# Kernel tuning notes

Hardware: AMD Instinct MI355X
Metric: run time of the kernel (lower is better)

## Reference

```python
import jax, jax.numpy as jnp
import numpy as np

NEG_SLOPE = 0.2  # DGL GATConv default leaky_relu slope
N_LIG, E_LIG = 10000, 80000
N_REC, E_REC = 30000, 480000
B = 32  # graphs per batch


def setup_inputs() -> dict:
    key = jax.random.key(0)
    ks = jax.random.split(key, 32)
    d = {}
    d["x_lig"] = jax.random.normal(ks[0], (N_LIG, 64), jnp.float32)
    d["src_lig"] = jax.random.randint(ks[1], (E_LIG,), 0, N_LIG, jnp.int32)
    d["dst_lig"] = jax.random.randint(ks[2], (E_LIG,), 0, N_LIG, jnp.int32)
    d["gid_lig"] = jnp.sort(jax.random.randint(ks[3], (N_LIG,), 0, B, jnp.int32))
    d["x_rec"] = jax.random.normal(ks[4], (N_REC, 64), jnp.float32)
    d["src_rec"] = jax.random.randint(ks[5], (E_REC,), 0, N_REC, jnp.int32)
    d["dst_rec"] = jax.random.randint(ks[6], (E_REC,), 0, N_REC, jnp.int32)
    d["gid_rec"] = jnp.sort(jax.random.randint(ks[7], (N_REC,), 0, B, jnp.int32))
    s = 0.1
    # GAT layer 1 (lig): 64 -> 10 heads x 64 ; layer 2: 64 -> 1 head x 128
    d["W1l"] = s * jax.random.normal(ks[8], (64, 10 * 64), jnp.float32)
    d["al1l"] = s * jax.random.normal(ks[9], (10, 64), jnp.float32)
    d["ar1l"] = s * jax.random.normal(ks[10], (10, 64), jnp.float32)
    d["b1l"] = jnp.zeros((10, 64), jnp.float32)
    d["W2l"] = s * jax.random.normal(ks[11], (64, 128), jnp.float32)
    d["al2l"] = s * jax.random.normal(ks[12], (1, 128), jnp.float32)
    d["ar2l"] = s * jax.random.normal(ks[13], (1, 128), jnp.float32)
    d["b2l"] = jnp.zeros((1, 128), jnp.float32)
    d["W1r"] = s * jax.random.normal(ks[14], (64, 10 * 64), jnp.float32)
    d["al1r"] = s * jax.random.normal(ks[15], (10, 64), jnp.float32)
    d["ar1r"] = s * jax.random.normal(ks[16], (10, 64), jnp.float32)
    d["b1r"] = jnp.zeros((10, 64), jnp.float32)
    d["W2r"] = s * jax.random.normal(ks[17], (64, 128), jnp.float32)
    d["al2r"] = s * jax.random.normal(ks[18], (1, 128), jnp.float32)
    d["ar2r"] = s * jax.random.normal(ks[19], (1, 128), jnp.float32)
    d["b2r"] = jnp.zeros((1, 128), jnp.float32)
    d["W_lin1"] = s * jax.random.normal(ks[20], (256, 128), jnp.float32)
    d["b_lin1"] = jnp.zeros((128,), jnp.float32)
    d["W_lin2"] = s * jax.random.normal(ks[21], (128, 1), jnp.float32)
    d["b_lin2"] = jnp.zeros((1,), jnp.float32)
    return d


def gat_conv(x, src, dst, W, al, ar, b, num_nodes):
    # DGL GATConv (eval mode: dropouts off). al/ar: [H, D]
    H, D = al.shape
    h = (x @ W).reshape(num_nodes, H, D)          # [N, H, D]
    el = jnp.einsum("nhd,hd->nh", h, al)          # [N, H]
    er = jnp.einsum("nhd,hd->nh", h, ar)
    e = jax.nn.leaky_relu(el[src] + er[dst], NEG_SLOPE)   # [E, H]
    # edge softmax over incoming edges of each dst node
    emax = jax.ops.segment_max(e, dst, num_segments=num_nodes)
    ex = jnp.exp(e - emax[dst])
    denom = jax.ops.segment_sum(ex, dst, num_segments=num_nodes)
    alpha = ex / denom[dst]                       # [E, H]
    msg = alpha[:, :, None] * h[src]              # [E, H, D]
    out = jax.ops.segment_sum(msg, dst, num_segments=num_nodes)
    return out + b[None]                          # [N, H, D]


def branch(x, src, dst, gid, W1, al1, ar1, b1, W2, al2, ar2, b2):
    n = x.shape[0]
    h = jax.nn.relu(gat_conv(x, src, dst, W1, al1, ar1, b1, n)).sum(axis=1)  # sum heads -> [N, 64]
    h = jax.nn.relu(gat_conv(h, src, dst, W2, al2, ar2, b2, n))[:, 0, :]     # [N, 128]
    return jax.ops.segment_max(h, gid, num_segments=B)                       # max readout [B, 128]


def reference(x_lig, src_lig, dst_lig, gid_lig, x_rec, src_rec, dst_rec, gid_rec,
              W1l, al1l, ar1l, b1l, W2l, al2l, ar2l, b2l,
              W1r, al1r, ar1r, b1r, W2r, al2r, ar2r, b2r,
              W_lin1, b_lin1, W_lin2, b_lin2):
    hlig = branch(x_lig, src_lig, dst_lig, gid_lig, W1l, al1l, ar1l, b1l, W2l, al2l, ar2l, b2l)
    hrec = branch(x_rec, src_rec, dst_rec, gid_rec, W1r, al1r, ar1r, b1r, W2r, al2r, ar2r, b2r)
    h = jnp.concatenate([hlig, hrec], axis=-1)    # [B, 256]
    h = jax.nn.relu(h @ W_lin1 + b_lin1)
    h = jax.nn.relu(h @ W_lin2 + b_lin2)
    return h.flatten()                            # [B]
```

## Files before the change

kernel.cpp:

```cpp
#include <hip/hip_runtime.h>

#define LRELU(x) fmaxf((x), 0.2f*(x))
#define ZPAD(f) ((f) + 4*((f)>>6))

static inline int cdiv(int a, int b) { return (a + b - 1) / b; }

template<int H, int DH>
__global__ void prep_wal2_kernel(const float* __restrict__ WA, const float* __restrict__ alA,
                                 const float* __restrict__ arA, float* __restrict__ walA,
                                 float* __restrict__ warA, int nbA,
                                 const float* __restrict__ WB, const float* __restrict__ alB,
                                 const float* __restrict__ arB, float* __restrict__ walB,
                                 float* __restrict__ warB) {
  constexpr int K = 64;
  constexpr int HD = H * DH;
  const float *W, *al, *ar; float *wal, *war; int bid;
  if (blockIdx.x < (unsigned)nbA) { W=WA; al=alA; ar=arA; wal=walA; war=warA; bid=blockIdx.x; }
  else { W=WB; al=alB; ar=arB; wal=walB; war=warB; bid=blockIdx.x-nbA; }
  const int wv = threadIdx.x >> 6, lane = threadIdx.x & 63;
  const int o = bid * (blockDim.x >> 6) + wv;
  if (o >= H * K) return;
  const int h = o / K, k = o - h * K;
  float pl = 0.f, pr = 0.f;
#pragma unroll
  for (int j = 0; j < DH / 64; j++) {
    int d = j * 64 + lane;
    float w = W[(size_t)k * HD + h * DH + d];
    pl += w * al[h * DH + d];
    pr += w * ar[h * DH + d];
  }
#pragma unroll
  for (int off = 32; off >= 1; off >>= 1) {
    pl += __shfl_xor(pl, off);
    pr += __shfl_xor(pr, off);
  }
  if (lane == 0) { wal[o] = pl; war[o] = pr; }
}

__global__ void elr10_2_kernel(const float* __restrict__ xA, const float* __restrict__ walA,
                               const float* __restrict__ warA, float* __restrict__ elA,
                               float* __restrict__ erA, int NA, int nbA,
                               const float* __restrict__ xB, const float* __restrict__ walB,
                               const float* __restrict__ warB, float* __restrict__ elB,
                               float* __restrict__ erB, int NB) {
  const float *x, *wal, *war; float *el, *er; int N, bid;
  if (blockIdx.x < (unsigned)nbA) { x=xA; wal=walA; war=warA; el=elA; er=erA; N=NA; bid=blockIdx.x; }
  else { x=xB; wal=walB; war=warB; el=elB; er=erB; N=NB; bid=blockIdx.x-nbA; }
  const int wv = threadIdx.x >> 6, lane = threadIdx.x & 63;
  const int n = bid * (blockDim.x >> 6) + wv;
  if (n >= N) return;
  const float xv = x[(size_t)n * 64 + lane];
#pragma unroll
  for (int h = 0; h < 10; h++) {
    float pl = xv * wal[h * 64 + lane];
    float pr = xv * war[h * 64 + lane];
#pragma unroll
    for (int off = 32; off >= 1; off >>= 1) {
      pl += __shfl_xor(pl, off);
      pr += __shfl_xor(pr, off);
    }
    if (lane == 0) { el[(size_t)n * 10 + h] = pl; er[(size_t)n * 10 + h] = pr; }
  }
}

__global__ void deg2_kernel(const int* __restrict__ dstA, int* __restrict__ degA, int EA, int nbA,
                            const int* __restrict__ dstB, int* __restrict__ degB, int EB) {
  const int* dst; int* deg; int E, t;
  if (blockIdx.x < (unsigned)nbA) { dst=dstA; deg=degA; E=EA; t=blockIdx.x*256+threadIdx.x; }
  else { dst=dstB; deg=degB; E=EB; t=(blockIdx.x-nbA)*256+threadIdx.x; }
  if (t < E) atomicAdd(&deg[dst[t]], 1);
}

__global__ void rowptr2_kernel(const int* __restrict__ degA, int* __restrict__ rpA,
                               int* __restrict__ curA, int* __restrict__ cntA, int NA, int nbA,
                               const int* __restrict__ degB, int* __restrict__ rpB,
                               int* __restrict__ curB, int* __restrict__ cntB, int NB) {
  const int* deg; int *rp, *cur, *cnt; int N, t;
  if (blockIdx.x < (unsigned)nbA) { deg=degA; rp=rpA; cur=curA; cnt=cntA; N=NA; t=blockIdx.x*256+threadIdx.x; }
  else { deg=degB; rp=rpB; cur=curB; cnt=cntB; N=NB; t=(blockIdx.x-nbA)*256+threadIdx.x; }
  int lane = threadIdx.x & 63;
  int v = (t < N) ? deg[t] : 0;
  int x = v;
#pragma unroll
  for (int off = 1; off < 64; off <<= 1) {
    int y = __shfl_up(x, off);
    if (lane >= off) x += y;
  }
  int total = __shfl(x, 63);
  int base = 0;
  if (lane == 0 && total > 0) base = atomicAdd(cnt, total);
  base = __shfl(base, 0);
  int excl = base + x - v;
  if (t < N) { rp[t] = excl; cur[t] = excl; }
}

__global__ void scatter_ex2_kernel(
    const int* __restrict__ srcA, const int* __restrict__ dstA, int* __restrict__ curA,
    int* __restrict__ outA, const float* __restrict__ elA, const float* __restrict__ erA,
    float* __restrict__ exA, int* __restrict__ eslotA, int EA, int nbA,
    const int* __restrict__ srcB, const int* __restrict__ dstB, int* __restrict__ curB,
    int* __restrict__ outB, const float* __restrict__ elB, const float* __restrict__ erB,
    float* __restrict__ exB, int* __restrict__ eslotB, int EB) {
  const int *src, *dst; int *cur, *out, *eslot; const float *el, *er; float *ex; int E, t;
  if (blockIdx.x < (unsigned)nbA) { src=srcA; dst=dstA; cur=curA; out=outA; el=elA; er=erA; ex=exA; eslot=eslotA; E=EA; t=blockIdx.x*256+threadIdx.x; }
  else { src=srcB; dst=dstB; cur=curB; out=outB; el=elB; er=erB; ex=exB; eslot=eslotB; E=EB; t=(blockIdx.x-nbA)*256+threadIdx.x; }
  if (t >= E) return;
  const int s = src[t], d = dst[t];
  const int slot = atomicAdd(&cur[d], 1);
  out[slot] = s;
  eslot[t] = slot;
  const float2* elv = (const float2*)el;
  const float2* erv = (const float2*)er;
  float2* exv = (float2*)ex;
#pragma unroll
  for (int j = 0; j < 5; j++) {
    float2 a = elv[(size_t)s * 5 + j];
    float2 b = erv[(size_t)d * 5 + j];
    float2 e;
    e.x = __expf(LRELU(a.x + b.x));
    e.y = __expf(LRELU(a.y + b.y));
    exv[(size_t)slot * 5 + j] = e;
  }
}

__global__ void ex2_2_kernel(const int* __restrict__ srcA, const int* __restrict__ dstA,
                             const int* __restrict__ eslotA, const float* __restrict__ el2A,
                             const float* __restrict__ er2A, float* __restrict__ ex2A,
                             int EA, int nbA,
                             const int* __restrict__ srcB, const int* __restrict__ dstB,
                             const int* __restrict__ eslotB, const float* __restrict__ el2B,
                             const float* __restrict__ er2B, float* __restrict__ ex2B, int EB) {
  const int *src, *dst, *eslot; const float *el2, *er2; float *ex2; int E, t;
  if (blockIdx.x < (unsigned)nbA) { src=srcA; dst=dstA; eslot=eslotA; el2=el2A; er2=er2A; ex2=ex2A; E=EA; t=blockIdx.x*256+threadIdx.x; }
  else { src=srcB; dst=dstB; eslot=eslotB; el2=el2B; er2=er2B; ex2=ex2B; E=EB; t=(blockIdx.x-nbA)*256+threadIdx.x; }
  if (t >= E) return;
  ex2[eslot[t]] = __expf(LRELU(el2[src[t]] + er2[dst[t]]));
}

__global__ void aggr_z10_2_kernel(const int* __restrict__ rpA, const int* __restrict__ degA,
                                  const int* __restrict__ srcsA, const float* __restrict__ xA,
                                  const float* __restrict__ exA, float* __restrict__ zA,
                                  int NA, int nbA,
                                  const int* __restrict__ rpB, const int* __restrict__ degB,
                                  const int* __restrict__ srcsB, const float* __restrict__ xB,
                                  const float* __restrict__ exB, float* __restrict__ zB, int NB) {
  const int *rp, *degp, *srcs; const float *x, *ex; float *z; int N, bid;
  if (blockIdx.x < (unsigned)nbA) { rp=rpA; degp=degA; srcs=srcsA; x=xA; ex=exA; z=zA; N=NA; bid=blockIdx.x; }
  else { rp=rpB; degp=degB; srcs=srcsB; x=xB; ex=exB; z=zB; N=NB; bid=blockIdx.x-nbA; }
  const int wv = threadIdx.x >> 6, lane = threadIdx.x & 63;
  const int n = bid * (blockDim.x >> 6) + wv;
  if (n >= N) return;
  const int beg = rp[n], dg = degp[n];
  const float2* exv = (const float2*)ex;
  float den[10], acc[10];
#pragma unroll
  for (int h = 0; h < 10; h++) { den[h] = 0.f; acc[h] = 0.f; }
  int i = 0;
  for (; i + 1 < dg; i += 2) {
    int s0 = srcs[beg + i], s1 = srcs[beg + i + 1];
    float xv0 = x[(size_t)s0 * 64 + lane];
    float xv1 = x[(size_t)s1 * 64 + lane];
    float e0[10], e1[10];
#pragma unroll
    for (int j = 0; j < 5; j++) {
      float2 a = exv[(size_t)(beg + i) * 5 + j];
      float2 c = exv[(size_t)(beg + i + 1) * 5 + j];
      e0[2 * j] = a.x; e0[2 * j + 1] = a.y;
      e1[2 * j] = c.x; e1[2 * j + 1] = c.y;
    }
#pragma unroll
    for (int h = 0; h < 10; h++) {
      den[h] += e0[h] + e1[h];
      acc[h] = fmaf(e0[h], xv0, fmaf(e1[h], xv1, acc[h]));
    }
  }
  if (i < dg) {
    int s0 = srcs[beg + i];
    float xv0 = x[(size_t)s0 * 64 + lane];
#pragma unroll
    for (int j = 0; j < 5; j++) {
      float2 a = exv[(size_t)(beg + i) * 5 + j];
      den[2 * j] += a.x;
      den[2 * j + 1] += a.y;
      acc[2 * j] = fmaf(a.x, xv0, acc[2 * j]);
      acc[2 * j + 1] = fmaf(a.y, xv0, acc[2 * j + 1]);
    }
  }
#pragma unroll
  for (int h = 0; h < 10; h++)
    z[(size_t)n * 640 + h * 64 + lane] = (dg > 0) ? acc[h] / den[h] : 0.f;
}

__global__ void aggr_z1_2_kernel(const int* __restrict__ rpA, const int* __restrict__ degA,
                                 const int* __restrict__ srcsA, const float* __restrict__ hA,
                                 const float* __restrict__ exA, float* __restrict__ zA,
                                 int NA, int nbA,
                                 const int* __restrict__ rpB, const int* __restrict__ degB,
                                 const int* __restrict__ srcsB, const float* __restrict__ hB,
                                 const float* __restrict__ exB, float* __restrict__ zB, int NB) {
  const int *rp, *degp, *srcs; const float *hin, *ex; float *z; int N, bid;
  if (blockIdx.x < (unsigned)nbA) { rp=rpA; degp=degA; srcs=srcsA; hin=hA; ex=exA; z=zA; N=NA; bid=blockIdx.x; }
  else { rp=rpB; degp=degB; srcs=srcsB; hin=hB; ex=exB; z=zB; N=NB; bid=blockIdx.x-nbA; }
  const int wv = threadIdx.x >> 6, lane = threadIdx.x & 63;
  const int n = bid * (blockDim.x >> 6) + wv;
  if (n >= N) return;
  const int beg = rp[n], dg = degp[n];
  float den = 0.f, acc = 0.f;
  int i = 0;
  for (; i + 1 < dg; i += 2) {
    int s0 = srcs[beg + i], s1 = srcs[beg + i + 1];
    float e0 = ex[beg + i], e1 = ex[beg + i + 1];
    den += e0 + e1;
    acc = fmaf(e0, hin[(size_t)s0 * 64 + lane], fmaf(e1, hin[(size_t)s1 * 64 + lane], acc));
  }
  if (i < dg) {
    int s0 = srcs[beg + i];
    float e0 = ex[beg + i];
    den += e0;
    acc = fmaf(e0, hin[(size_t)s0 * 64 + lane], acc);
  }
  z[(size_t)n * 64 + lane] = (dg > 0) ? acc / den : 0.f;
}

__global__ void gemm_sumheads2_kernel(
    const float* __restrict__ zA, const float* __restrict__ WA, const float* __restrict__ bA,
    const float* __restrict__ wal2A, const float* __restrict__ war2A, float* __restrict__ h1A,
    float* __restrict__ el2A, float* __restrict__ er2A, int NA, int nbA,
    const float* __restrict__ zB, const float* __restrict__ WB, const float* __restrict__ bB,
    const float* __restrict__ wal2B, const float* __restrict__ war2B, float* __restrict__ h1B,
    float* __restrict__ el2B, float* __restrict__ er2B, int NB) {
  constexpr int NPB = 16;
  __shared__ float zs[NPB][680];
  const float *z, *W, *bb, *wal2, *war2; float *h1sum, *el2, *er2; int N, tile;
  if (blockIdx.x < (unsigned)nbA) { z=zA; W=WA; bb=bA; wal2=wal2A; war2=war2A; h1sum=h1A; el2=el2A; er2=er2A; N=NA; tile=blockIdx.x; }
  else { z=zB; W=WB; bb=bB; wal2=wal2B; war2=war2B; h1sum=h1B; el2=el2B; er2=er2B; N=NB; tile=blockIdx.x-nbA; }
  const int f = threadIdx.x;
  const int n0 = tile * NPB;
  const int pf = ZPAD(f);
#pragma unroll
  for (int i = 0; i < NPB; i++) {
    int n = n0 + i;
    zs[i][pf] = (n < N) ? z[(size_t)n * 640 + f] : 0.f;
  }
  __syncthreads();
  const int f4 = f % 160;
  const int ng = f / 160;
  const int head = f4 >> 4;
  const int base = 68 * head;
  float acc[4][4];
#pragma unroll
  for (int i = 0; i < 4; i++)
#pragma unroll
    for (int j = 0; j < 4; j++) acc[i][j] = 0.f;
  const float4* W4 = (const float4*)W;
  float4 wn[4];
#pragma unroll
  for (int j = 0; j < 4; j++) wn[j] = W4[(size_t)j * 160 + f4];
#pragma unroll
  for (int k4 = 0; k4 < 16; k4++) {
    float4 wc[4];
#pragma unroll
    for (int j = 0; j < 4; j++) wc[j] = wn[j];
    if (k4 < 15) {
#pragma unroll
      for (int j = 0; j < 4; j++) wn[j] = W4[(size_t)(4 * (k4 + 1) + j) * 160 + f4];
    }
    float4 zq[4];
#pragma unroll
    for (int i = 0; i < 4; i++)
      zq[i] = *(const float4*)&zs[ng * 4 + i][base + 4 * k4];
#pragma unroll
    for (int j4 = 0; j4 < 4; j4++) {
      const float4 w4 = wc[j4];
#pragma unroll
      for (int i = 0; i < 4; i++) {
        const float zv = j4 == 0 ? zq[i].x : j4 == 1 ? zq[i].y : j4 == 2 ? zq[i].z : zq[i].w;
        acc[i][0] = fmaf(zv, w4.x, acc[i][0]);
        acc[i][1] = fmaf(zv, w4.y, acc[i][1]);
        acc[i][2] = fmaf(zv, w4.z, acc[i][2]);
        acc[i][3] = fmaf(zv, w4.w, acc[i][3]);
      }
    }
  }
  const float4 b4 = ((const float4*)bb)[f4];
  __syncthreads();
#pragma unroll
  for (int i = 0; i < 4; i++) {
    float* row = &zs[ng * 4 + i][ZPAD(4 * f4)];
    row[0] = fmaxf(acc[i][0] + b4.x, 0.f);
    row[1] = fmaxf(acc[i][1] + b4.y, 0.f);
    row[2] = fmaxf(acc[i][2] + b4.z, 0.f);
    row[3] = fmaxf(acc[i][3] + b4.w, 0.f);
  }
  __syncthreads();
  const int lane = threadIdx.x & 63;
  for (int idx = threadIdx.x; idx < NPB * 64; idx += 640) {
    const int i = idx >> 6, d = idx & 63;
    float s = 0.f;
#pragma unroll
    for (int h = 0; h < 10; h++) s += zs[i][68 * h + d];
    const int n = n0 + i;
    float pl = s * wal2[d], pr = s * war2[d];
#pragma unroll
    for (int off = 32; off >= 1; off >>= 1) {
      pl += __shfl_xor(pl, off);
      pr += __shfl_xor(pr, off);
    }
    if (n < N) {
      h1sum[(size_t)n * 64 + d] = s;
      if (lane == 0) { el2[n] = pl; er2[n] = pr; }
    }
  }
}

__global__ void gemm2_readout3_kernel(
    const float* __restrict__ zA, const float* __restrict__ WA, const float* __restrict__ bA,
    const int* __restrict__ gidA, int NA, int coA, int nbA,
    const float* __restrict__ zB, const float* __restrict__ WB, const float* __restrict__ bB,
    const int* __restrict__ gidB, int NB, int coB,
    float* __restrict__ readout) {
  constexpr int NPB = 16;
  __shared__ float zs[NPB][64];
  __shared__ float vals[NPB][128];
  __shared__ int gids[NPB];
  const float *z, *W, *bb; const int* gid; int N, colOff, tile;
  if (blockIdx.x < (unsigned)nbA) { z=zA; W=WA; bb=bA; gid=gidA; N=NA; colOff=coA; tile=blockIdx.x; }
  else { z=zB; W=WB; bb=bB; gid=gidB; N=NB; colOff=coB; tile=blockIdx.x-nbA; }
  const int f = threadIdx.x;
  const int n0 = tile * NPB;
  for (int idx = f; idx < NPB * 64; idx += 128) {
    int i = idx >> 6, k = idx & 63;
    int n = n0 + i;
    zs[i][k] = (n < N) ? z[(size_t)n * 64 + k] : 0.f;
  }
  if (f < NPB) gids[f] = (n0 + f < N) ? gid[n0 + f] : -1;
  __syncthreads();
  float acc[NPB];
#pragma unroll
  for (int i = 0; i < NPB; i++) acc[i] = 0.f;
#pragma unroll 4
  for (int k4 = 0; k4 < 16; k4++) {
    const float w0 = W[(size_t)(4 * k4 + 0) * 128 + f];
    const float w1 = W[(size_t)(4 * k4 + 1) * 128 + f];
    const float w2 = W[(size_t)(4 * k4 + 2) * 128 + f];
    const float w3 = W[(size_t)(4 * k4 + 3) * 128 + f];
#pragma unroll
    for (int i = 0; i < NPB; i++) {
      float4 zq = *(const float4*)&zs[i][4 * k4];
      acc[i] = fmaf(zq.x, w0, fmaf(zq.y, w1, fmaf(zq.z, w2, fmaf(zq.w, w3, acc[i]))));
    }
  }
  const float bbf = bb[f];
#pragma unroll
  for (int i = 0; i < NPB; i++) vals[i][f] = fmaxf(acc[i] + bbf, 0.f);
  __syncthreads();
  float run = 0.f;
  int curg = -1;
#pragma unroll
  for (int i = 0; i < NPB; i++) {
    int g = gids[i];
    if (g < 0) break;
    if (g != curg) {
      if (curg >= 0)
        atomicMax((unsigned int*)&readout[curg * 256 + colOff + f], __float_as_uint(run));
      curg = g;
      run = 0.f;
    }
    run = fmaxf(run, vals[i][f]);
  }
  if (curg >= 0)
    atomicMax((unsigned int*)&readout[curg * 256 + colOff + f], __float_as_uint(run));
}

__global__ void mlp_kernel(const float* __restrict__ readout, const float* __restrict__ W1,
                           const float* __restrict__ b1, const float* __restrict__ W2,
                           const float* __restrict__ b2, float* __restrict__ out) {
  int b = blockIdx.x;
  int j = threadIdx.x;
  __shared__ float rs[256];
  rs[j] = readout[b * 256 + j];
  rs[j + 128] = readout[b * 256 + 128 + j];
  __syncthreads();
  float acc = b1[j];
#pragma unroll 8
  for (int k = 0; k < 256; k++) acc += rs[k] * W1[k * 128 + j];
  acc = fmaxf(acc, 0.f);
  float p = acc * W2[j];
#pragma unroll
  for (int off = 32; off >= 1; off >>= 1) p += __shfl_xor(p, off);
  __shared__ float wsum[2];
  if ((threadIdx.x & 63) == 0) wsum[threadIdx.x >> 6] = p;
  __syncthreads();
  if (threadIdx.x == 0) {
    float s = wsum[0] + wsum[1] + b2[0];
    out[b] = fmaxf(s, 0.f);
  }
}

extern "C" void kernel_launch(void* const* d_in, const int* in_sizes, int n_in,
                              void* d_out, int out_size, void* d_ws, size_t ws_size,
                              hipStream_t stream) {
  const float* x_lig = (const float*)d_in[0];
  const int* src_lig = (const int*)d_in[1];
  const int* dst_lig = (const int*)d_in[2];
  const int* gid_lig = (const int*)d_in[3];
  const float* x_rec = (const float*)d_in[4];
  const int* src_rec = (const int*)d_in[5];
  const int* dst_rec = (const int*)d_in[6];
  const int* gid_rec = (const int*)d_in[7];
  const float* W1l = (const float*)d_in[8];
  const float* al1l = (const float*)d_in[9];
  const float* ar1l = (const float*)d_in[10];
  const float* b1l = (const float*)d_in[11];
  const float* W2l = (const float*)d_in[12];
  const float* al2l = (const float*)d_in[13];
  const float* ar2l = (const float*)d_in[14];
  const float* b2l = (const float*)d_in[15];
  const float* W1r = (const float*)d_in[16];
  const float* al1r = (const float*)d_in[17];
  const float* ar1r = (const float*)d_in[18];
  const float* b1r = (const float*)d_in[19];
  const float* W2r = (const float*)d_in[20];
  const float* al2r = (const float*)d_in[21];
  const float* ar2r = (const float*)d_in[22];
  const float* b2r = (const float*)d_in[23];
  const float* W_lin1 = (const float*)d_in[24];
  const float* b_lin1 = (const float*)d_in[25];
  const float* W_lin2 = (const float*)d_in[26];
  const float* b_lin2 = (const float*)d_in[27];

  const int NL = 10000, EL = 80000, NR = 30000, ER = 480000;
  float* p = (float*)d_ws;
  float* zL = p;      p += (size_t)NL * 640;
  float* zR = p;      p += (size_t)NR * 640;
  float* ex1L = p;    p += (size_t)EL * 10;
  float* ex1R = p;    p += (size_t)ER * 10;
  float* ex2L = p;    p += EL;
  float* ex2R = p;    p += ER;
  float* z2L = p;     p += (size_t)NL * 64;
  float* z2R = p;     p += (size_t)NR * 64;
  float* h1L = p;     p += (size_t)NL * 64;
  float* h1R = p;     p += (size_t)NR * 64;
  float* el1L = p;    p += (size_t)NL * 10;
  float* er1L = p;    p += (size_t)NL * 10;
  float* el1R = p;    p += (size_t)NR * 10;
  float* er1R = p;    p += (size_t)NR * 10;
  float* el2L = p;    p += NL;
  float* er2L = p;    p += NL;
  float* el2R = p;    p += NR;
  float* er2R = p;    p += NR;
  float* wal1l = p;   p += 640;
  float* war1l = p;   p += 640;
  float* wal1r = p;   p += 640;
  float* war1r = p;   p += 640;
  float* wal2l = p;   p += 64;
  float* war2l = p;   p += 64;
  float* wal2r = p;   p += 64;
  float* war2r = p;   p += 64;
  float* zero_base = p;
  float* readout = p; p += 32 * 256;
  int* ip = (int*)p;
  int* degL = ip;     ip += NL;
  int* cntL = ip;     ip += 1;
  int* degR = ip;     ip += NR;
  int* cntR = ip;     ip += 1;
  size_t zero_bytes = (size_t)((char*)ip - (char*)zero_base);
  int* rpL = ip;      ip += NL;
  int* curL = ip;     ip += NL;
  int* srcsL = ip;    ip += EL;
  int* rpR = ip;      ip += NR;
  int* curR = ip;     ip += NR;
  int* srcsR = ip;    ip += ER;
  int* eslotL = ip;   ip += EL;
  int* eslotR = ip;   ip += ER;

  hipMemsetAsync(zero_base, 0, zero_bytes, stream);

  prep_wal2_kernel<10, 64><<<160, 512, 0, stream>>>(W1l, al1l, ar1l, wal1l, war1l, 80,
                                                    W1r, al1r, ar1r, wal1r, war1r);
  prep_wal2_kernel<1, 128><<<16, 512, 0, stream>>>(W2l, al2l, ar2l, wal2l, war2l, 8,
                                                   W2r, al2r, ar2r, wal2r, war2r);
  deg2_kernel<<<cdiv(EL, 256) + cdiv(ER, 256), 256, 0, stream>>>(
      dst_lig, degL, EL, cdiv(EL, 256), dst_rec, degR, ER);
  rowptr2_kernel<<<cdiv(NL, 256) + cdiv(NR, 256), 256, 0, stream>>>(
      degL, rpL, curL, cntL, NL, cdiv(NL, 256), degR, rpR, curR, cntR, NR);
  elr10_2_kernel<<<cdiv(NL, 4) + cdiv(NR, 4), 256, 0, stream>>>(
      x_lig, wal1l, war1l, el1L, er1L, NL, cdiv(NL, 4),
      x_rec, wal1r, war1r, el1R, er1R, NR);
  scatter_ex2_kernel<<<cdiv(EL, 256) + cdiv(ER, 256), 256, 0, stream>>>(
      src_lig, dst_lig, curL, srcsL, el1L, er1L, ex1L, eslotL, EL, cdiv(EL, 256),
      src_rec, dst_rec, curR, srcsR, el1R, er1R, ex1R, eslotR, ER);
  aggr_z10_2_kernel<<<cdiv(NL, 8) + cdiv(NR, 8), 512, 0, stream>>>(
      rpL, degL, srcsL, x_lig, ex1L, zL, NL, cdiv(NL, 8),
      rpR, degR, srcsR, x_rec, ex1R, zR, NR);
  gemm_sumheads2_kernel<<<cdiv(NL, 16) + cdiv(NR, 16), 640, 0, stream>>>(
      zL, W1l, b1l, wal2l, war2l, h1L, el2L, er2L, NL, cdiv(NL, 16),
      zR, W1r, b1r, wal2r, war2r, h1R, el2R, er2R, NR);
  ex2_2_kernel<<<cdiv(EL, 256) + cdiv(ER, 256), 256, 0, stream>>>(
      src_lig, dst_lig, eslotL, el2L, er2L, ex2L, EL, cdiv(EL, 256),
      src_rec, dst_rec, eslotR, el2R, er2R, ex2R, ER);
  aggr_z1_2_kernel<<<cdiv(NL, 8) + cdiv(NR, 8), 512, 0, stream>>>(
      rpL, degL, srcsL, h1L, ex2L, z2L, NL, cdiv(NL, 8),
      rpR, degR, srcsR, h1R, ex2R, z2R, NR);
  gemm2_readout3_kernel<<<cdiv(NL, 16) + cdiv(NR, 16), 128, 0, stream>>>(
      z2L, W2l, b2l, gid_lig, NL, 0, cdiv(NL, 16),
      z2R, W2r, b2r, gid_rec, NR, 128, readout);

  mlp_kernel<<<32, 128, 0, stream>>>(readout, W_lin1, b_lin1, W_lin2, b_lin2, (float*)d_out);
}
```

Baseline: 480.1 us.

## Fuse edge aggregation into per-layer GEMM kernels via shared memory

Merges the layer-1 neighbor aggregation into the head-projection GEMM kernel, and the layer-2 aggregation into the GEMM-plus-max-readout kernel. Aggregated node features now go straight into shared memory instead of a global z buffer, which removes a large write and re-read (about 100 MB for layer 1) and two kernel launches. In exchange, the 10 waves of a 640-thread block must cover 16 nodes, so some waves aggregate two nodes and others one. That imbalance and the serial gather-then-GEMM inside each block may lower latency hiding.

```diff
diff --git a/kernel.cpp b/kernel.cpp
--- a/kernel.cpp
+++ b/kernel.cpp
@@ -137,121 +137,86 @@
   ex2[eslot[t]] = __expf(LRELU(el2[src[t]] + er2[dst[t]]));
 }
 
-__global__ void aggr_z10_2_kernel(const int* __restrict__ rpA, const int* __restrict__ degA,
-                                  const int* __restrict__ srcsA, const float* __restrict__ xA,
-                                  const float* __restrict__ exA, float* __restrict__ zA,
-                                  int NA, int nbA,
-                                  const int* __restrict__ rpB, const int* __restrict__ degB,
-                                  const int* __restrict__ srcsB, const float* __restrict__ xB,
-                                  const float* __restrict__ exB, float* __restrict__ zB, int NB) {
-  const int *rp, *degp, *srcs; const float *x, *ex; float *z; int N, bid;
-  if (blockIdx.x < (unsigned)nbA) { rp=rpA; degp=degA; srcs=srcsA; x=xA; ex=exA; z=zA; N=NA; bid=blockIdx.x; }
-  else { rp=rpB; degp=degB; srcs=srcsB; x=xB; ex=exB; z=zB; N=NB; bid=blockIdx.x-nbA; }
-  const int wv = threadIdx.x >> 6, lane = threadIdx.x & 63;
-  const int n = bid * (blockDim.x >> 6) + wv;
-  if (n >= N) return;
-  const int beg = rp[n], dg = degp[n];
-  const float2* exv = (const float2*)ex;
-  float den[10], acc[10];
-#pragma unroll
-  for (int h = 0; h < 10; h++) { den[h] = 0.f; acc[h] = 0.f; }
-  int i = 0;
-  for (; i + 1 < dg; i += 2) {
-    int s0 = srcs[beg + i], s1 = srcs[beg + i + 1];
-    float xv0 = x[(size_t)s0 * 64 + lane];
-    float xv1 = x[(size_t)s1 * 64 + lane];
-    float e0[10], e1[10];
-#pragma unroll
-    for (int j = 0; j < 5; j++) {
-      float2 a = exv[(size_t)(beg + i) * 5 + j];
-      float2 c = exv[(size_t)(beg + i + 1) * 5 + j];
-      e0[2 * j] = a.x; e0[2 * j + 1] = a.y;
-      e1[2 * j] = c.x; e1[2 * j + 1] = c.y;
-    }
-#pragma unroll
-    for (int h = 0; h < 10; h++) {
-      den[h] += e0[h] + e1[h];
-      acc[h] = fmaf(e0[h], xv0, fmaf(e1[h], xv1, acc[h]));
-    }
-  }
-  if (i < dg) {
-    int s0 = srcs[beg + i];
-    float xv0 = x[(size_t)s0 * 64 + lane];
-#pragma unroll
-    for (int j = 0; j < 5; j++) {
-      float2 a = exv[(size_t)(beg + i) * 5 + j];
-      den[2 * j] += a.x;
-      den[2 * j + 1] += a.y;
-      acc[2 * j] = fmaf(a.x, xv0, acc[2 * j]);
-      acc[2 * j + 1] = fmaf(a.y, xv0, acc[2 * j + 1]);
-    }
-  }
-#pragma unroll
-  for (int h = 0; h < 10; h++)
-    z[(size_t)n * 640 + h * 64 + lane] = (dg > 0) ? acc[h] / den[h] : 0.f;
-}
-
-__global__ void aggr_z1_2_kernel(const int* __restrict__ rpA, const int* __restrict__ degA,
-                                 const int* __restrict__ srcsA, const float* __restrict__ hA,
-                                 const float* __restrict__ exA, float* __restrict__ zA,
-                                 int NA, int nbA,
-                                 const int* __restrict__ rpB, const int* __restrict__ degB,
-                                 const int* __restrict__ srcsB, const float* __restrict__ hB,
-                                 const float* __restrict__ exB, float* __restrict__ zB, int NB) {
-  const int *rp, *degp, *srcs; const float *hin, *ex; float *z; int N, bid;
-  if (blockIdx.x < (unsigned)nbA) { rp=rpA; degp=degA; srcs=srcsA; hin=hA; ex=exA; z=zA; N=NA; bid=blockIdx.x; }
-  else { rp=rpB; degp=degB; srcs=srcsB; hin=hB; ex=exB; z=zB; N=NB; bid=blockIdx.x-nbA; }
-  const int wv = threadIdx.x >> 6, lane = threadIdx.x & 63;
-  const int n = bid * (blockDim.x >> 6) + wv;
-  if (n >= N) return;
-  const int beg = rp[n], dg = degp[n];
-  float den = 0.f, acc = 0.f;
-  int i = 0;
-  for (; i + 1 < dg; i += 2) {
-    int s0 = srcs[beg + i], s1 = srcs[beg + i + 1];
-    float e0 = ex[beg + i], e1 = ex[beg + i + 1];
-    den += e0 + e1;
-    acc = fmaf(e0, hin[(size_t)s0 * 64 + lane], fmaf(e1, hin[(size_t)s1 * 64 + lane], acc));
-  }
-  if (i < dg) {
-    int s0 = srcs[beg + i];
-    float e0 = ex[beg + i];
-    den += e0;
-    acc = fmaf(e0, hin[(size_t)s0 * 64 + lane], acc);
-  }
-  z[(size_t)n * 64 + lane] = (dg > 0) ? acc / den : 0.f;
-}
-
-__global__ void gemm_sumheads2_kernel(
-    const float* __restrict__ zA, const float* __restrict__ WA, const float* __restrict__ bA,
-    const float* __restrict__ wal2A, const float* __restrict__ war2A, float* __restrict__ h1A,
-    float* __restrict__ el2A, float* __restrict__ er2A, int NA, int nbA,
-    const float* __restrict__ zB, const float* __restrict__ WB, const float* __restrict__ bB,
-    const float* __restrict__ wal2B, const float* __restrict__ war2B, float* __restrict__ h1B,
-    float* __restrict__ el2B, float* __restrict__ er2B, int NB) {
+__global__ void aggr_gemm1_kernel(
+    const int* __restrict__ rpA, const int* __restrict__ degA, const int* __restrict__ srcsA,
+    const float* __restrict__ xA, const float* __restrict__ exA,
+    const float* __restrict__ WA, const float* __restrict__ bA,
+    const float* __restrict__ wal2A, const float* __restrict__ war2A,
+    float* __restrict__ h1A, float* __restrict__ el2A, float* __restrict__ er2A, int NA, int nbA,
+    const int* __restrict__ rpB, const int* __restrict__ degB, const int* __restrict__ srcsB,
+    const float* __restrict__ xB, const float* __restrict__ exB,
+    const float* __restrict__ WB, const float* __restrict__ bB,
+    const float* __restrict__ wal2B, const float* __restrict__ war2B,
+    float* __restrict__ h1B, float* __restrict__ el2B, float* __restrict__ er2B, int NB) {
   constexpr int NPB = 16;
   __shared__ float zs[NPB][680];
-  const float *z, *W, *bb, *wal2, *war2; float *h1sum, *el2, *er2; int N, tile;
-  if (blockIdx.x < (unsigned)nbA) { z=zA; W=WA; bb=bA; wal2=wal2A; war2=war2A; h1sum=h1A; el2=el2A; er2=er2A; N=NA; tile=blockIdx.x; }
-  else { z=zB; W=WB; bb=bB; wal2=wal2B; war2=war2B; h1sum=h1B; el2=el2B; er2=er2B; N=NB; tile=blockIdx.x-nbA; }
+  const int *rp, *degp, *srcs; const float *x, *ex, *W, *bb, *wal2, *war2;
+  float *h1sum, *el2, *er2; int N, tile;
+  if (blockIdx.x < (unsigned)nbA) {
+    rp=rpA; degp=degA; srcs=srcsA; x=xA; ex=exA; W=WA; bb=bA; wal2=wal2A; war2=war2A;
+    h1sum=h1A; el2=el2A; er2=er2A; N=NA; tile=blockIdx.x;
+  } else {
+    rp=rpB; degp=degB; srcs=srcsB; x=xB; ex=exB; W=WB; bb=bB; wal2=wal2B; war2=war2B;
+    h1sum=h1B; el2=el2B; er2=er2B; N=NB; tile=blockIdx.x-nbA;
+  }
   const int f = threadIdx.x;
+  const int wv = f >> 6, lane = f & 63;
   const int n0 = tile * NPB;
-  const int pf = ZPAD(f);
-#pragma unroll
-  for (int i = 0; i < NPB; i++) {
-    int n = n0 + i;
-    zs[i][pf] = (n < N) ? z[(size_t)n * 640 + f] : 0.f;
+  const float2* exv = (const float2*)ex;
+  for (int ni = wv; ni < NPB; ni += 10) {
+    const int n = n0 + ni;
+    float den[10], acc[10];
+#pragma unroll
+    for (int h = 0; h < 10; h++) { den[h] = 0.f; acc[h] = 0.f; }
+    int dg = 0;
+    if (n < N) {
+      const int beg = rp[n];
+      dg = degp[n];
+      int i = 0;
+      for (; i + 1 < dg; i += 2) {
+        int s0 = srcs[beg + i], s1 = srcs[beg + i + 1];
+        float xv0 = x[(size_t)s0 * 64 + lane];
+        float xv1 = x[(size_t)s1 * 64 + lane];
+        float e0[10], e1[10];
+#pragma unroll
+        for (int j = 0; j < 5; j++) {
+          float2 a = exv[(size_t)(beg + i) * 5 + j];
+          float2 c = exv[(size_t)(beg + i + 1) * 5 + j];
+          e0[2 * j] = a.x; e0[2 * j + 1] = a.y;
+          e1[2 * j] = c.x; e1[2 * j + 1] = c.y;
+        }
+#pragma unroll
+        for (int h = 0; h < 10; h++) {
+          den[h] += e0[h] + e1[h];
+          acc[h] = fmaf(e0[h], xv0, fmaf(e1[h], xv1, acc[h]));
+        }
+      }
+      if (i < dg) {
+        float xv0 = x[(size_t)srcs[beg + i] * 64 + lane];
+#pragma unroll
+        for (int j = 0; j < 5; j++) {
+          float2 a = exv[(size_t)(beg + i) * 5 + j];
+          den[2 * j] += a.x;
+          den[2 * j + 1] += a.y;
+          acc[2 * j] = fmaf(a.x, xv0, acc[2 * j]);
+          acc[2 * j + 1] = fmaf(a.y, xv0, acc[2 * j + 1]);
+        }
+      }
+    }
+#pragma unroll
+    for (int h = 0; h < 10; h++)
+      zs[ni][68 * h + lane] = (dg > 0) ? acc[h] / den[h] : 0.f;
   }
   __syncthreads();
   const int f4 = f % 160;
   const int ng = f / 160;
   const int head = f4 >> 4;
   const int base = 68 * head;
-  float acc[4][4];
+  float acc2[4][4];
 #pragma unroll
   for (int i = 0; i < 4; i++)
 #pragma unroll
-    for (int j = 0; j < 4; j++) acc[i][j] = 0.f;
+    for (int j = 0; j < 4; j++) acc2[i][j] = 0.f;
   const float4* W4 = (const float4*)W;
   float4 wn[4];
 #pragma unroll
@@ -275,10 +240,10 @@
 #pragma unroll
       for (int i = 0; i < 4; i++) {
         const float zv = j4 == 0 ? zq[i].x : j4 == 1 ? zq[i].y : j4 == 2 ? zq[i].z : zq[i].w;
-        acc[i][0] = fmaf(zv, w4.x, acc[i][0]);
-        acc[i][1] = fmaf(zv, w4.y, acc[i][1]);
-        acc[i][2] = fmaf(zv, w4.z, acc[i][2]);
-        acc[i][3] = fmaf(zv, w4.w, acc[i][3]);
+        acc2[i][0] = fmaf(zv, w4.x, acc2[i][0]);
+        acc2[i][1] = fmaf(zv, w4.y, acc2[i][1]);
+        acc2[i][2] = fmaf(zv, w4.z, acc2[i][2]);
+        acc2[i][3] = fmaf(zv, w4.w, acc2[i][3]);
       }
     }
   }
@@ -287,13 +252,12 @@
 #pragma unroll
   for (int i = 0; i < 4; i++) {
     float* row = &zs[ng * 4 + i][ZPAD(4 * f4)];
-    row[0] = fmaxf(acc[i][0] + b4.x, 0.f);
-    row[1] = fmaxf(acc[i][1] + b4.y, 0.f);
-    row[2] = fmaxf(acc[i][2] + b4.z, 0.f);
-    row[3] = fmaxf(acc[i][3] + b4.w, 0.f);
-  }
-  __syncthreads();
-  const int lane = threadIdx.x & 63;
+    row[0] = fmaxf(acc2[i][0] + b4.x, 0.f);
+    row[1] = fmaxf(acc2[i][1] + b4.y, 0.f);
+    row[2] = fmaxf(acc2[i][2] + b4.z, 0.f);
+    row[3] = fmaxf(acc2[i][3] + b4.w, 0.f);
+  }
+  __syncthreads();
   for (int idx = threadIdx.x; idx < NPB * 64; idx += 640) {
     const int i = idx >> 6, d = idx & 63;
     float s = 0.f;
@@ -313,63 +277,94 @@
   }
 }
 
-__global__ void gemm2_readout3_kernel(
-    const float* __restrict__ zA, const float* __restrict__ WA, const float* __restrict__ bA,
+__global__ void aggr_gemm2_readout_kernel(
+    const int* __restrict__ rpA, const int* __restrict__ degA, const int* __restrict__ srcsA,
+    const float* __restrict__ hA, const float* __restrict__ exA,
+    const float* __restrict__ WA, const float* __restrict__ bA,
     const int* __restrict__ gidA, int NA, int coA, int nbA,
-    const float* __restrict__ zB, const float* __restrict__ WB, const float* __restrict__ bB,
+    const int* __restrict__ rpB, const int* __restrict__ degB, const int* __restrict__ srcsB,
+    const float* __restrict__ hB, const float* __restrict__ exB,
+    const float* __restrict__ WB, const float* __restrict__ bB,
     const int* __restrict__ gidB, int NB, int coB,
     float* __restrict__ readout) {
   constexpr int NPB = 16;
   __shared__ float zs[NPB][64];
   __shared__ float vals[NPB][128];
   __shared__ int gids[NPB];
-  const float *z, *W, *bb; const int* gid; int N, colOff, tile;
-  if (blockIdx.x < (unsigned)nbA) { z=zA; W=WA; bb=bA; gid=gidA; N=NA; colOff=coA; tile=blockIdx.x; }
-  else { z=zB; W=WB; bb=bB; gid=gidB; N=NB; colOff=coB; tile=blockIdx.x-nbA; }
+  const int *rp, *degp, *srcs; const float *hin, *ex, *W, *bb; const int* gid;
+  int N, colOff, tile;
+  if (blockIdx.x < (unsigned)nbA) {
+    rp=rpA; degp=degA; srcs=srcsA; hin=hA; ex=exA; W=WA; bb=bA; gid=gidA;
+    N=NA; colOff=coA; tile=blockIdx.x;
+  } else {
+    rp=rpB; degp=degB; srcs=srcsB; hin=hB; ex=exB; W=WB; bb=bB; gid=gidB;
+    N=NB; colOff=coB; tile=blockIdx.x-nbA;
+  }
   const int f = threadIdx.x;
+  const int wv = f >> 6, lane = f & 63;
   const int n0 = tile * NPB;
-  for (int idx = f; idx < NPB * 64; idx += 128) {
-    int i = idx >> 6, k = idx & 63;
-    int n = n0 + i;
-    zs[i][k] = (n < N) ? z[(size_t)n * 64 + k] : 0.f;
+  for (int ni = wv; ni < NPB; ni += 4) {
+    const int n = n0 + ni;
+    float den = 0.f, acc = 0.f;
+    int dg = 0;
+    if (n < N) {
+      const int beg = rp[n];
+      dg = degp[n];
+      int i = 0;
+      for (; i + 1 < dg; i += 2) {
+        int s0 = srcs[beg + i], s1 = srcs[beg + i + 1];
+        float e0 = ex[beg + i], e1 = ex[beg + i + 1];
+        den += e0 + e1;
+        acc = fmaf(e0, hin[(size_t)s0 * 64 + lane], fmaf(e1, hin[(size_t)s1 * 64 + lane], acc));
+      }
+      if (i < dg) {
+        float e0 = ex[beg + i];
+        den += e0;
+        acc = fmaf(e0, hin[(size_t)srcs[beg + i] * 64 + lane], acc);
+      }
+    }
+    zs[ni][lane] = (dg > 0) ? acc / den : 0.f;
   }
   if (f < NPB) gids[f] = (n0 + f < N) ? gid[n0 + f] : -1;
   __syncthreads();
-  float acc[NPB];
-#pragma unroll
-  for (int i = 0; i < NPB; i++) acc[i] = 0.f;
+  const int col = f & 127, nb = f >> 7;
+  float acc8[8];
+#pragma unroll
+  for (int i = 0; i < 8; i++) acc8[i] = 0.f;
 #pragma unroll 4
   for (int k4 = 0; k4 < 16; k4++) {
-    const float w0 = W[(size_t)(4 * k4 + 0) * 128 + f];
-    const float w1 = W[(size_t)(4 * k4 + 1) * 128 + f];
-    const float w2 = W[(size_t)(4 * k4 + 2) * 128 + f];
-    const float w3 = W[(size_t)(4 * k4 + 3) * 128 + f];
+    const float w0 = W[(size_t)(4 * k4 + 0) * 128 + col];
+    const float w1 = W[(size_t)(4 * k4 + 1) * 128 + col];
+    const float w2 = W[(size_t)(4 * k4 + 2) * 128 + col];
+    const float w3 = W[(size_t)(4 * k4 + 3) * 128 + col];
+#pragma unroll
+    for (int i = 0; i < 8; i++) {
+      float4 zq = *(const float4*)&zs[nb * 8 + i][4 * k4];
+      acc8[i] = fmaf(zq.x, w0, fmaf(zq.y, w1, fmaf(zq.z, w2, fmaf(zq.w, w3, acc8[i]))));
+    }
+  }
+  const float bbf = bb[col];
+#pragma unroll
+  for (int i = 0; i < 8; i++) vals[nb * 8 + i][col] = fmaxf(acc8[i] + bbf, 0.f);
+  __syncthreads();
+  if (f < 128) {
+    float run = 0.f;
+    int curg = -1;
 #pragma unroll
     for (int i = 0; i < NPB; i++) {
-      float4 zq = *(const float4*)&zs[i][4 * k4];
-      acc[i] = fmaf(zq.x, w0, fmaf(zq.y, w1, fmaf(zq.z, w2, fmaf(zq.w, w3, acc[i]))));
-    }
-  }
-  const float bbf = bb[f];
-#pragma unroll
-  for (int i = 0; i < NPB; i++) vals[i][f] = fmaxf(acc[i] + bbf, 0.f);
-  __syncthreads();
-  float run = 0.f;
-  int curg = -1;
-#pragma unroll
-  for (int i = 0; i < NPB; i++) {
-    int g = gids[i];
-    if (g < 0) break;
-    if (g != curg) {
-      if (curg >= 0)
-        atomicMax((unsigned int*)&readout[curg * 256 + colOff + f], __float_as_uint(run));
-      curg = g;
-      run = 0.f;
-    }
-    run = fmaxf(run, vals[i][f]);
-  }
-  if (curg >= 0)
-    atomicMax((unsigned int*)&readout[curg * 256 + colOff + f], __float_as_uint(run));
+      int g = gids[i];
+      if (g < 0) break;
+      if (g != curg) {
+        if (curg >= 0)
+          atomicMax((unsigned int*)&readout[curg * 256 + colOff + f], __float_as_uint(run));
+        curg = g;
+        run = 0.f;
+      }
+      run = fmaxf(run, vals[i][f]);
+    }
+    if (curg >= 0)
+      atomicMax((unsigned int*)&readout[curg * 256 + colOff + f], __float_as_uint(run));
+  }
 }
 
 __global__ void mlp_kernel(const float* __restrict__ readout, const float* __restrict__ W1,
@@ -431,14 +426,10 @@
 
   const int NL = 10000, EL = 80000, NR = 30000, ER = 480000;
   float* p = (float*)d_ws;
-  float* zL = p;      p += (size_t)NL * 640;
-  float* zR = p;      p += (size_t)NR * 640;
   float* ex1L = p;    p += (size_t)EL * 10;
   float* ex1R = p;    p += (size_t)ER * 10;
   float* ex2L = p;    p += EL;
   float* ex2R = p;    p += ER;
-  float* z2L = p;     p += (size_t)NL * 64;
-  float* z2R = p;     p += (size_t)NR * 64;
   float* h1L = p;     p += (size_t)NL * 64;
   float* h1R = p;     p += (size_t)NR * 64;
   float* el1L = p;    p += (size_t)NL * 10;
@@ -490,21 +481,15 @@
   scatter_ex2_kernel<<<cdiv(EL, 256) + cdiv(ER, 256), 256, 0, stream>>>(
       src_lig, dst_lig, curL, srcsL, el1L, er1L, ex1L, eslotL, EL, cdiv(EL, 256),
       src_rec, dst_rec, curR, srcsR, el1R, er1R, ex1R, eslotR, ER);
-  aggr_z10_2_kernel<<<cdiv(NL, 8) + cdiv(NR, 8), 512, 0, stream>>>(
-      rpL, degL, srcsL, x_lig, ex1L, zL, NL, cdiv(NL, 8),
-      rpR, degR, srcsR, x_rec, ex1R, zR, NR);
-  gemm_sumheads2_kernel<<<cdiv(NL, 16) + cdiv(NR, 16), 640, 0, stream>>>(
-      zL, W1l, b1l, wal2l, war2l, h1L, el2L, er2L, NL, cdiv(NL, 16),
-      zR, W1r, b1r, wal2r, war2r, h1R, el2R, er2R, NR);
+  aggr_gemm1_kernel<<<cdiv(NL, 16) + cdiv(NR, 16), 640, 0, stream>>>(
+      rpL, degL, srcsL, x_lig, ex1L, W1l, b1l, wal2l, war2l, h1L, el2L, er2L, NL, cdiv(NL, 16),
+      rpR, degR, srcsR, x_rec, ex1R, W1r, b1r, wal2r, war2r, h1R, el2R, er2R, NR);
   ex2_2_kernel<<<cdiv(EL, 256) + cdiv(ER, 256), 256, 0, stream>>>(
       src_lig, dst_lig, eslotL, el2L, er2L, ex2L, EL, cdiv(EL, 256),
       src_rec, dst_rec, eslotR, el2R, er2R, ex2R, ER);
-  aggr_z1_2_kernel<<<cdiv(NL, 8) + cdiv(NR, 8), 512, 0, stream>>>(
-      rpL, degL, srcsL, h1L, ex2L, z2L, NL, cdiv(NL, 8),
-      rpR, degR, srcsR, h1R, ex2R, z2R, NR);
-  gemm2_readout3_kernel<<<cdiv(NL, 16) + cdiv(NR, 16), 128, 0, stream>>>(
-      z2L, W2l, b2l, gid_lig, NL, 0, cdiv(NL, 16),
-      z2R, W2r, b2r, gid_rec, NR, 128, readout);
+  aggr_gemm2_readout_kernel<<<cdiv(NL, 16) + cdiv(NR, 16), 256, 0, stream>>>(
+      rpL, degL, srcsL, h1L, ex2L, W2l, b2l, gid_lig, NL, 0, cdiv(NL, 16),
+      rpR, degR, srcsR, h1R, ex2R, W2r, b2r, gid_rec, NR, 128, readout);
 
   mlp_kernel<<<32, 128, 0, stream>>>(readout, W_lin1, b_lin1, W_lin2, b_lin2, (float*)d_out);
 }
```

After: 475.9 us. No clear change (-0.9%).
